# Kernel tuning notes

Hardware: AMD Instinct MI355X
Metric: run time of the kernel (lower is better)

The kernel has to match this reference:

```python
import jax, jax.numpy as jnp
import numpy as np

B, S, E, H = 2, 4096, 768, 12
D = E // H  # head_dim = 64
SCALE = D ** -0.5
NEG = -1e9


def setup_inputs() -> dict:
    key = jax.random.key(0)
    ks = jax.random.split(key, 10)
    init = lambda k, shape: jax.random.normal(k, shape, dtype=jnp.float32) * (shape[-1] ** -0.5)
    x = jax.random.normal(ks[0], (B, S, E), dtype=jnp.float32)
    attention_mask = jnp.zeros((B, 1, S, S), dtype=jnp.float32)
    # additive causal mask: 0 on/below diagonal, -1e9 above
    causal = jnp.where(jnp.tril(jnp.ones((S, S), dtype=bool)), 0.0, NEG).astype(jnp.float32)
    causal_attention_mask = causal[None, None]
    return {
        "x": x,
        "attention_mask": attention_mask,
        "causal_attention_mask": causal_attention_mask,
        "Wq": init(ks[1], (E, E)), "bq": jnp.zeros((E,), jnp.float32),
        "Wk": init(ks[2], (E, E)), "bk": jnp.zeros((E,), jnp.float32),
        "Wv": init(ks[3], (E, E)), "bv": jnp.zeros((E,), jnp.float32),
        "Wo": init(ks[4], (E, E)), "bo": jnp.zeros((E,), jnp.float32),
    }


def _split_heads(t):
    # [B,S,E] -> [B,H,S,D]
    return t.reshape(B, S, H, D).transpose(0, 2, 1, 3)


def reference(x, attention_mask, causal_attention_mask, Wq, bq, Wk, bk, Wv, bv, Wo, bo):
    q = _split_heads(x @ Wq.T + bq)
    k = _split_heads(x @ Wk.T + bk)
    v = _split_heads(x @ Wv.T + bv)
    mask = attention_mask + causal_attention_mask  # [B,1,S,S]
    scores = jnp.einsum("bhqd,bhkd->bhqk", q, k) * SCALE + mask
    probs = jax.nn.softmax(scores.astype(jnp.float32), axis=-1).astype(q.dtype)
    out = jnp.einsum("bhqk,bhkd->bhqd", probs, v)
    out = out.transpose(0, 2, 1, 3).reshape(B, S, E)
    return out @ Wo.T + bo
```

## Files before the change

kernel.cpp:

```cpp
#include <hip/hip_runtime.h>
#include <hip/hip_bf16.h>
#include <stdint.h>

#define B_ 2
#define S_ 4096
#define E_ 768
#define H_ 12
#define D_ 64
#define M_TOT (B_*S_)
#define NQKV (3*E_)

typedef __attribute__((ext_vector_type(8)))  short bf16x8;
typedef __attribute__((ext_vector_type(4)))  float f32x4;
typedef __attribute__((ext_vector_type(16))) float f32x16;
typedef unsigned short u16;
typedef unsigned int   u32;

__device__ __forceinline__ u16 f2bf(float f) {
  __hip_bfloat16 h = __float2bfloat16(f);
  return *reinterpret_cast<u16*>(&h);
}

__device__ __forceinline__ float bf2f(u16 u) {
  union { u32 i; float f; } v; v.i = ((u32)u) << 16; return v.f;
}

__device__ __forceinline__ u32 cvtpk(float lo, float hi) {
  u32 r;
  asm("v_cvt_pk_bf16_f32 %0, %1, %2" : "=v"(r) : "v"(lo), "v"(hi));
  return r;
}

#define GLDS(gp, lp) __builtin_amdgcn_global_load_lds( \
    (const __attribute__((address_space(1))) void*)(gp), \
    (__attribute__((address_space(3))) void*)(lp), 16, 0, 0)

#define QSCALE 0.1803368801111573f


__global__ void k_cast_x(const float* __restrict__ x, u16* __restrict__ xb) {
  int i = blockIdx.x * blockDim.x + threadIdx.x;
  float4 v = reinterpret_cast<const float4*>(x)[i];
  ushort4 o;
  o.x = f2bf(v.x); o.y = f2bf(v.y); o.z = f2bf(v.z); o.w = f2bf(v.w);
  reinterpret_cast<ushort4*>(xb)[i] = o;
}

__global__ void k_pack_wqkv(const float* __restrict__ Wq, const float* __restrict__ Wk,
                            const float* __restrict__ Wv, const float* __restrict__ bq,
                            const float* __restrict__ bk, const float* __restrict__ bv,
                            u16* __restrict__ wqkv, float* __restrict__ bqkv) {
  int i = blockIdx.x * blockDim.x + threadIdx.x;
  int base = i * 4;
  int n = base / E_;
  int k = base % E_;
  const float* src; float sc;
  if (n < E_)        { src = Wq + (size_t)n*E_ + k;        sc = QSCALE; }
  else if (n < 2*E_) { src = Wk + (size_t)(n-E_)*E_ + k;   sc = 1.f; }
  else               { src = Wv + (size_t)(n-2*E_)*E_ + k; sc = 1.f; }
  float4 v = *reinterpret_cast<const float4*>(src);
  ushort4 o;
  o.x = f2bf(v.x*sc); o.y = f2bf(v.y*sc); o.z = f2bf(v.z*sc); o.w = f2bf(v.w*sc);
  reinterpret_cast<ushort4*>(wqkv)[i] = o;
  if (i < NQKV) {
    float b = (i < E_) ? bq[i]*QSCALE : (i < 2*E_) ? bk[i-E_] : bv[i-2*E_];
    bqkv[i] = b;
  }
}

__global__ void k_cast_wo(const float* __restrict__ Wo, u16* __restrict__ wo) {
  int i = blockIdx.x * blockDim.x + threadIdx.x;
  float4 v = reinterpret_cast<const float4*>(Wo)[i];
  ushort4 o;
  o.x = f2bf(v.x); o.y = f2bf(v.y); o.z = f2bf(v.z); o.w = f2bf(v.w);
  reinterpret_cast<ushort4*>(wo)[i] = o;
}


template<int MODE>
__global__ __launch_bounds__(256)
void k_gemm(const u16* __restrict__ A, const u16* __restrict__ W,
            const float* __restrict__ bias,
            u16* __restrict__ dq, u16* __restrict__ dk, u16* __restrict__ dv,
            float* __restrict__ fout)
{
  constexpr int BN = (MODE == 0) ? 128 : 64;
  constexpr int NF = BN / 32;
  __shared__ u16 As[128*64];
  __shared__ u16 Ws[BN*64];
  const int tid  = threadIdx.x;
  const int lane = tid & 63, wave = tid >> 6;
  const int m0 = blockIdx.x * 128;
  const int n0 = blockIdx.y * BN;
  const int g  = lane >> 4, cc = lane & 15;
  const int wr = (wave >> 1) * 64, wc = (wave & 1) * (BN/2);
  const int srow = lane >> 3;
  const int scol = (lane & 7) * 8;

  f32x4 acc[4][NF];
  #pragma unroll
  for (int m = 0; m < 4; ++m)
    #pragma unroll
    for (int n = 0; n < NF; ++n) acc[m][n] = (f32x4){0.f,0.f,0.f,0.f};

  for (int k0 = 0; k0 < E_; k0 += 64) {
    __syncthreads();
    #pragma unroll
    for (int i = 0; i < 4; ++i) {
      const int r0 = (i*4 + wave) * 8;
      GLDS(A + (size_t)(m0 + r0 + srow)*E_ + k0 + scol, As + r0*64);
    }
    #pragma unroll
    for (int i = 0; i < BN/32; ++i) {
      const int r0 = (i*4 + wave) * 8;
      GLDS(W + (size_t)(n0 + r0 + srow)*E_ + k0 + scol, Ws + r0*64);
    }
    __syncthreads();
    #pragma unroll
    for (int kk = 0; kk < 64; kk += 32) {
      bf16x8 af[4], bfr[NF];
      #pragma unroll
      for (int m = 0; m < 4; ++m)
        af[m] = *reinterpret_cast<const bf16x8*>(As + (wr + m*16 + cc)*64 + kk + g*8);
      #pragma unroll
      for (int n = 0; n < NF; ++n)
        bfr[n] = *reinterpret_cast<const bf16x8*>(Ws + (wc + n*16 + cc)*64 + kk + g*8);
      #pragma unroll
      for (int m = 0; m < 4; ++m)
        #pragma unroll
        for (int n = 0; n < NF; ++n)
          acc[m][n] = __builtin_amdgcn_mfma_f32_16x16x32_bf16(af[m], bfr[n], acc[m][n], 0, 0, 0);
    }
  }

  #pragma unroll
  for (int n = 0; n < NF; ++n) {
    const int colg = n0 + wc + n*16 + cc;
    const float bb = bias[colg];
    if (MODE == 0) {
      const int which = colg / E_;
      const int nn = colg % E_;
      const int h = nn >> 6, d = nn & 63;
      #pragma unroll
      for (int m = 0; m < 4; ++m)
        #pragma unroll
        for (int j = 0; j < 4; ++j) {
          const int row = m0 + wr + m*16 + g*4 + j;
          const int b = row >> 12, s = row & (S_-1);
          const u16 val = f2bf(acc[m][n][j] + bb);
          if (which == 0)       dq[(((size_t)b*H_ + h)*S_ + s)*D_ + d] = val;
          else if (which == 1)  dk[(((size_t)b*H_ + h)*S_ + s)*D_ + d] = val;
          else                  dv[(((size_t)b*H_ + h)*D_ + d)*S_ + s] = val;
        }
    } else {
      #pragma unroll
      for (int m = 0; m < 4; ++m)
        #pragma unroll
        for (int j = 0; j < 4; ++j) {
          const int row = m0 + wr + m*16 + g*4 + j;
          fout[(size_t)row*E_ + colg] = acc[m][n][j] + bb;
        }
    }
  }
}


__global__ __launch_bounds__(256, 3)
void k_attn(const u16* __restrict__ Qb, const u16* __restrict__ Kb,
            const u16* __restrict__ Vtg, u16* __restrict__ AO,
            u16* __restrict__ PO, float2* __restrict__ PML)
{
  __shared__ u16 Ks[2][32*128];
  __shared__ u16 Vs[2][32*128];
  const int tid = threadIdx.x, lane = tid & 63, w = tid >> 6;

  const int L    = blockIdx.x;
  const int slot = L >> 8;
  const int cu   = L & 255;
  const int x    = cu & 7;
  const int c    = cu >> 3;
  int r;
  if (slot < 4) r = slot*32 + ((slot & 1) ? (31 - c) : c);
  else          r = 128 + c;
  int head, qt, mode;
  if (r < 120) {
    const int g_ = r / 15, o = r % 15;
    if (o < 9) {
      if (o < 3) { head = o; qt = 15 - g_; mode = 0; }
      else { const int hh = o - 3; head = hh >> 1; mode = 1 + (hh & 1); qt = 31 - 2*g_; }
    } else { const int hh = o - 9; head = hh >> 1; mode = 1 + (hh & 1); qt = 30 - 2*g_; }
  } else {
    const int rr = r - 120; qt = 7 - rr/3; head = rr % 3; mode = 0;
  }
  const int bh = x*3 + head;
  const int q0 = qt * 128;
  const int nt = (mode == 0) ? (2*qt + 2) : (qt + 1);
  const int kvtb = (mode == 2) ? (qt + 1) : 0;

  const size_t kbase = (size_t)bh * S_ * D_;
  const size_t vbase = (size_t)bh * D_ * S_;
  const int hi = lane >> 5, l31 = lane & 31;
  const int swz = (lane & 15) << 4;
  const int qg = q0 + w*32 + l31;

  int stA[2], stB[2];
  #pragma unroll
  for (int i = 0; i < 2; ++i) {
    const int jj = 2*w + i;
    const int row = jj*4 + (lane >> 4);
    const int gb = ((lane & 15) * 16) ^ ((row & 15) << 4);
    stA[i] = row + 32*(gb >> 7);
    stB[i] = (gb & 127) >> 1;
  }

  bf16x8 qf[4];
  #pragma unroll
  for (int ds = 0; ds < 4; ++ds)
    qf[ds] = *reinterpret_cast<const bf16x8*>(Qb + kbase + (size_t)qg*D_ + ds*16 + hi*8);

  const bf16x8 ones = {(short)0x3F80, (short)0x3F80, (short)0x3F80, (short)0x3F80,
                       (short)0x3F80, (short)0x3F80, (short)0x3F80, (short)0x3F80};

  float m_run = 0.f;
  f32x16 o0, o1, cin, lacc;
  #pragma unroll
  for (int r2 = 0; r2 < 16; ++r2) { o0[r2] = 0.f; o1[r2] = 0.f; cin[r2] = 0.f; lacc[r2] = 0.f; }

#define STAGE(buf, kv0_) do { \
    _Pragma("unroll") \
    for (int i = 0; i < 2; ++i) { \
      GLDS(Kb  + kbase + (size_t)((kv0_) + stA[i])*D_ + stB[i], &Ks[buf][(2*w+i)*512]); \
      GLDS(Vtg + vbase + (size_t)stA[i]*S_ + (kv0_) + stB[i],   &Vs[buf][(2*w+i)*512]); \
    } } while(0)

  int cur = 0;
  STAGE(0, kvtb*64);

  for (int it = 0; it < nt; ++it) {
    asm volatile("s_waitcnt vmcnt(0)" ::: "memory");
    __builtin_amdgcn_s_barrier();
    asm volatile("" ::: "memory");
    if (it + 1 < nt) STAGE(cur ^ 1, (kvtb + it + 1)*64);

    const int kvt = kvtb + it;
    const int kv0 = kvt * 64;
    const u16* bK = Ks[cur];
    const u16* bV = Vs[cur];

    f32x16 s0, s1;
    __builtin_amdgcn_s_setprio(1);
    {
      const int off = (16*hi ^ swz) >> 1;
      bf16x8 a0 = *reinterpret_cast<const bf16x8*>(bK + l31*128 + off);
      bf16x8 a1 = *reinterpret_cast<const bf16x8*>(bK + l31*128 + (off ^ 64));
      s0 = __builtin_amdgcn_mfma_f32_32x32x16_bf16(a0, qf[0], cin, 0, 0, 0);
      s1 = __builtin_amdgcn_mfma_f32_32x32x16_bf16(a1, qf[0], cin, 0, 0, 0);
    }
    #pragma unroll
    for (int ds = 1; ds < 4; ++ds) {
      const int off = ((32*ds + 16*hi) ^ swz) >> 1;
      bf16x8 a0 = *reinterpret_cast<const bf16x8*>(bK + l31*128 + off);
      bf16x8 a1 = *reinterpret_cast<const bf16x8*>(bK + l31*128 + (off ^ 64));
      s0 = __builtin_amdgcn_mfma_f32_32x32x16_bf16(a0, qf[ds], s0, 0, 0, 0);
      s1 = __builtin_amdgcn_mfma_f32_32x32x16_bf16(a1, qf[ds], s1, 0, 0, 0);
    }
    __builtin_amdgcn_s_setprio(0);

    if (kvt >= 2*qt) {
      #pragma unroll
      for (int r2 = 0; r2 < 16; ++r2) {
        const int kvl = kv0 + (r2&3) + 8*(r2>>2) + 4*hi;
        s0[r2] = (kvl      > qg) ? -1e30f : s0[r2];
        s1[r2] = (kvl + 32 > qg) ? -1e30f : s1[r2];
      }
    }

    #pragma unroll
    for (int r2 = 0; r2 < 16; ++r2) s0[r2] = exp2f(s0[r2]);
    #pragma unroll
    for (int r2 = 0; r2 < 16; ++r2) s1[r2] = exp2f(s1[r2]);

    u32 c16[16];
    #pragma unroll
    for (int i = 0; i < 8; ++i) {
      c16[i]   = cvtpk(s0[2*i], s0[2*i+1]);
      c16[8+i] = cvtpk(s1[2*i], s1[2*i+1]);
    }

    #pragma unroll
    for (int ks = 0; ks < 4; ++ks) {
      const int cb = (ks>>1)*8 + (ks&1)*4;
      u32 x0 = c16[cb],   y0 = c16[cb+2];
      u32 x1 = c16[cb+1], y1 = c16[cb+3];
      asm volatile("v_permlane32_swap_b32 %0, %1" : "+v"(x0), "+v"(y0));
      asm volatile("v_permlane32_swap_b32 %0, %1" : "+v"(x1), "+v"(y1));
      union { u32 u[4]; bf16x8 v; } pf;
      pf.u[0] = x0; pf.u[1] = x1; pf.u[2] = y0; pf.u[3] = y1;
      const int voff = ((32*ks + 16*hi) ^ swz) >> 1;
      bf16x8 v0 = *reinterpret_cast<const bf16x8*>(bV + l31*128 + voff);
      bf16x8 v1 = *reinterpret_cast<const bf16x8*>(bV + l31*128 + (voff ^ 64));
      __builtin_amdgcn_s_setprio(1);
      o0   = __builtin_amdgcn_mfma_f32_32x32x16_bf16(v0,   pf.v, o0,   0, 0, 0);
      o1   = __builtin_amdgcn_mfma_f32_32x32x16_bf16(v1,   pf.v, o1,   0, 0, 0);
      lacc = __builtin_amdgcn_mfma_f32_32x32x16_bf16(ones, pf.v, lacc, 0, 0, 0);
      __builtin_amdgcn_s_setprio(0);
    }

    if (!__all(lacc[0] <= 1073741824.0f)) {
      const float alpha = 0x1p-40f;
      m_run += 40.f;
      #pragma unroll
      for (int r2 = 0; r2 < 16; ++r2) {
        o0[r2] *= alpha; o1[r2] *= alpha; lacc[r2] *= alpha;
        cin[r2] -= 40.f;
      }
    }

    cur ^= 1;
  }
#undef STAGE

  const float l_run = lacc[0];
  if (mode == 0) {
    const int b = bh / H_, h = bh % H_;
    const float inv = 1.0f / l_run;
    u16* dst = AO + ((size_t)b*S_ + qg)*E_ + h*64;
    #pragma unroll
    for (int aa = 0; aa < 4; ++aa) {
      ushort4 wv;
      wv.x = f2bf(o0[4*aa+0]*inv); wv.y = f2bf(o0[4*aa+1]*inv);
      wv.z = f2bf(o0[4*aa+2]*inv); wv.w = f2bf(o0[4*aa+3]*inv);
      *reinterpret_cast<ushort4*>(dst + aa*8 + hi*4) = wv;
    }
    #pragma unroll
    for (int aa = 0; aa < 4; ++aa) {
      ushort4 wv;
      wv.x = f2bf(o1[4*aa+0]*inv); wv.y = f2bf(o1[4*aa+1]*inv);
      wv.z = f2bf(o1[4*aa+2]*inv); wv.w = f2bf(o1[4*aa+3]*inv);
      *reinterpret_cast<ushort4*>(dst + 32 + aa*8 + hi*4) = wv;
    }
  } else {
    const int qslot = (bh*16 + (qt-16))*2 + (mode - 1);
    const int rowt = w*32 + l31;
    u16* po = PO + (size_t)qslot*(128*64) + rowt*64;
    #pragma unroll
    for (int aa = 0; aa < 4; ++aa) {
      ushort4 wv;
      wv.x = f2bf(o0[4*aa+0]); wv.y = f2bf(o0[4*aa+1]);
      wv.z = f2bf(o0[4*aa+2]); wv.w = f2bf(o0[4*aa+3]);
      *reinterpret_cast<ushort4*>(po + aa*8 + hi*4) = wv;
    }
    #pragma unroll
    for (int aa = 0; aa < 4; ++aa) {
      ushort4 wv;
      wv.x = f2bf(o1[4*aa+0]); wv.y = f2bf(o1[4*aa+1]);
      wv.z = f2bf(o1[4*aa+2]); wv.w = f2bf(o1[4*aa+3]);
      *reinterpret_cast<ushort4*>(po + 32 + aa*8 + hi*4) = wv;
    }
    if (hi == 0) PML[qslot*128 + rowt] = make_float2(m_run, l_run);
  }
}


__global__ __launch_bounds__(256)
void k_comb(const u16* __restrict__ PO, const float2* __restrict__ PML,
            u16* __restrict__ AO)
{
  const int bid = blockIdx.x;
  const int bh = bid >> 4, qi = bid & 15, q = 16 + qi;
  const int t = threadIdx.x;
  const int r = t >> 1, half = t & 1;
  const int s0 = (bh*16 + qi)*2, s1 = s0 + 1;
  const float2 ml0 = PML[s0*128 + r];
  const float2 ml1 = PML[s1*128 + r];
  const float mstar = fmaxf(ml0.x, ml1.x);
  const float w0 = exp2f(ml0.x - mstar);
  const float w1 = exp2f(ml1.x - mstar);
  const float inv = 1.0f / (ml0.y*w0 + ml1.y*w1);
  const float a0 = w0 * inv, a1 = w1 * inv;
  const u16* p0 = PO + (size_t)s0*(128*64) + r*64 + half*32;
  const u16* p1 = PO + (size_t)s1*(128*64) + r*64 + half*32;
  const int b = bh / H_, h = bh % H_;
  const int row = q*128 + r;
  u16* dst = AO + ((size_t)b*S_ + row)*E_ + h*64 + half*32;
  #pragma unroll
  for (int i = 0; i < 4; ++i) {
    bf16x8 v0 = *reinterpret_cast<const bf16x8*>(p0 + i*8);
    bf16x8 v1 = *reinterpret_cast<const bf16x8*>(p1 + i*8);
    ushort4 lo, hi4;
    float f0 = bf2f(((const u16*)&v0)[0])*a0 + bf2f(((const u16*)&v1)[0])*a1;
    float f1 = bf2f(((const u16*)&v0)[1])*a0 + bf2f(((const u16*)&v1)[1])*a1;
    float f2 = bf2f(((const u16*)&v0)[2])*a0 + bf2f(((const u16*)&v1)[2])*a1;
    float f3 = bf2f(((const u16*)&v0)[3])*a0 + bf2f(((const u16*)&v1)[3])*a1;
    lo.x = f2bf(f0); lo.y = f2bf(f1); lo.z = f2bf(f2); lo.w = f2bf(f3);
    float f4 = bf2f(((const u16*)&v0)[4])*a0 + bf2f(((const u16*)&v1)[4])*a1;
    float f5 = bf2f(((const u16*)&v0)[5])*a0 + bf2f(((const u16*)&v1)[5])*a1;
    float f6 = bf2f(((const u16*)&v0)[6])*a0 + bf2f(((const u16*)&v1)[6])*a1;
    float f7 = bf2f(((const u16*)&v0)[7])*a0 + bf2f(((const u16*)&v1)[7])*a1;
    hi4.x = f2bf(f4); hi4.y = f2bf(f5); hi4.z = f2bf(f6); hi4.w = f2bf(f7);
    *reinterpret_cast<ushort4*>(dst + i*8)     = lo;
    *reinterpret_cast<ushort4*>(dst + i*8 + 4) = hi4;
  }
}


extern "C" void kernel_launch(void* const* d_in, const int* in_sizes, int n_in,
                              void* d_out, int out_size, void* d_ws, size_t ws_size,
                              hipStream_t stream) {
  const float* x  = (const float*)d_in[0];
  const float* Wq = (const float*)d_in[3];
  const float* bq = (const float*)d_in[4];
  const float* Wk = (const float*)d_in[5];
  const float* bk = (const float*)d_in[6];
  const float* Wv = (const float*)d_in[7];
  const float* bv = (const float*)d_in[8];
  const float* Wo = (const float*)d_in[9];
  const float* bo = (const float*)d_in[10];
  float* out = (float*)d_out;

  const size_t SZ_X   = (size_t)M_TOT * E_ * 2;
  const size_t SZ_WQKV= (size_t)NQKV * E_ * 2;
  const size_t SZ_WO  = (size_t)E_ * E_ * 2;
  const size_t SZ_B   = (size_t)NQKV * 4;
  char* w = (char*)d_ws;
  u16*   xb   = (u16*)(w);
  u16*   wqkv = (u16*)(w + SZ_X);
  u16*   wob  = (u16*)(w + SZ_X + SZ_WQKV);
  float* bqkv = (float*)(w + SZ_X + SZ_WQKV + SZ_WO);
  char*  w2   = w + SZ_X + SZ_WQKV + SZ_WO + SZ_B;
  u16* Qb = (u16*)(w2);
  u16* Kb = (u16*)(w2 + SZ_X);
  u16* Vb = (u16*)(w2 + 2*SZ_X);
  u16* AO = (u16*)(w2 + 3*SZ_X);
  u16* PO = xb;
  float2* PML = (float2*)(w2 + 4*SZ_X);

  k_cast_x  <<<6144, 256, 0, stream>>>(x, xb);
  k_pack_wqkv<<<1728, 256, 0, stream>>>(Wq, Wk, Wv, bq, bk, bv, wqkv, bqkv);
  k_cast_wo <<<576,  256, 0, stream>>>(Wo, wob);

  dim3 gq(64, 18);
  k_gemm<0><<<gq, 256, 0, stream>>>(xb, wqkv, bqkv, Qb, Kb, Vb, nullptr);

  k_attn<<<1152, 256, 0, stream>>>(Qb, Kb, Vb, AO, PO, PML);
  k_comb<<<384, 256, 0, stream>>>(PO, PML, AO);

  dim3 go(64, 12);
  k_gemm<1><<<go, 256, 0, stream>>>(AO, wob, bo, nullptr, nullptr, nullptr, out);
}
```

Before: 201.9 us.

## Use stream-K style equal-work partitioning for causal attention blocks

```diff
diff --git a/kernel.cpp b/kernel.cpp
--- a/kernel.cpp
+++ b/kernel.cpp
@@ -168,84 +168,84 @@
 __global__ __launch_bounds__(256, 3)
 void k_attn(const u16* __restrict__ Qb, const u16* __restrict__ Kb,
             const u16* __restrict__ Vtg, u16* __restrict__ AO,
-            u16* __restrict__ PO, float2* __restrict__ PML)
+            u16* __restrict__ PO, float2* __restrict__ PMLA,
+            float2* __restrict__ PMLB)
 {
   __shared__ u16 Ks[2][32*128];
   __shared__ u16 Vs[2][32*128];
-  const int tid = threadIdx.x, lane = tid & 63, w = tid >> 6;
-
-  const int L    = blockIdx.x;
-  const int slot = L >> 8;
-  const int cu   = L & 255;
-  const int x    = cu & 7;
-  const int c    = cu >> 3;
-  int r;
-  if (slot < 4) r = slot*32 + ((slot & 1) ? (31 - c) : c);
-  else          r = 128 + c;
-  int head, qt, mode;
-  if (r < 120) {
-    const int g_ = r / 15, o = r % 15;
-    if (o < 9) {
-      if (o < 3) { head = o; qt = 15 - g_; mode = 0; }
-      else { const int hh = o - 3; head = hh >> 1; mode = 1 + (hh & 1); qt = 31 - 2*g_; }
-    } else { const int hh = o - 9; head = hh >> 1; mode = 1 + (hh & 1); qt = 30 - 2*g_; }
-  } else {
-    const int rr = r - 120; qt = 7 - rr/3; head = rr % 3; mode = 0;
-  }
-  const int bh = x*3 + head;
-  const int q0 = qt * 128;
-  const int nt = (mode == 0) ? (2*qt + 2) : (qt + 1);
-  const int kvtb = (mode == 2) ? (qt + 1) : 0;
+  const int tid = threadIdx.x, lane = tid & 63, wv = tid >> 6;
+
+  const int L  = blockIdx.x;
+  const int x  = L & 7;
+  const int g  = L >> 3;
+  const int h  = g >> 5;
+  const int qh = g & 31;
+  const int bh = x*3 + h;
+  const int b_ = bh / H_, h_ = bh % H_;
 
   const size_t kbase = (size_t)bh * S_ * D_;
   const size_t vbase = (size_t)bh * D_ * S_;
   const int hi = lane >> 5, l31 = lane & 31;
   const int swz = (lane & 15) << 4;
-  const int qg = q0 + w*32 + l31;
 
   int stA[2], stB[2];
   #pragma unroll
   for (int i = 0; i < 2; ++i) {
-    const int jj = 2*w + i;
+    const int jj = 2*wv + i;
     const int row = jj*4 + (lane >> 4);
     const int gb = ((lane & 15) * 16) ^ ((row & 15) << 4);
     stA[i] = row + 32*(gb >> 7);
     stB[i] = (gb & 127) >> 1;
   }
 
-  bf16x8 qf[4];
-  #pragma unroll
-  for (int ds = 0; ds < 4; ++ds)
-    qf[ds] = *reinterpret_cast<const bf16x8*>(Qb + kbase + (size_t)qg*D_ + ds*16 + hi*8);
+  const int lw0 = 33*qh;
+  int qt = (int)((sqrtf(4.0f*lw0 + 1.0f) - 1.0f) * 0.5f);
+  while ((qt+1)*(qt+2) <= lw0) ++qt;
+  while (qt*qt + qt > lw0) --qt;
+  int kv = lw0 - (qt*qt + qt);
+  bool headSeg = (kv == 0);
 
   const bf16x8 ones = {(short)0x3F80, (short)0x3F80, (short)0x3F80, (short)0x3F80,
                        (short)0x3F80, (short)0x3F80, (short)0x3F80, (short)0x3F80};
 
-  float m_run = 0.f;
+  bf16x8 qf[4];
+  float m_run;
   f32x16 o0, o1, cin, lacc;
-  #pragma unroll
-  for (int r2 = 0; r2 < 16; ++r2) { o0[r2] = 0.f; o1[r2] = 0.f; cin[r2] = 0.f; lacc[r2] = 0.f; }
-
-#define STAGE(buf, kv0_) do { \
+
+#define LOADQ(qtc) do { \
+    const int qg_ = (qtc)*128 + wv*32 + l31; \
+    _Pragma("unroll") \
+    for (int ds = 0; ds < 4; ++ds) \
+      qf[ds] = *reinterpret_cast<const bf16x8*>(Qb + kbase + (size_t)qg_*D_ + ds*16 + hi*8); \
+    m_run = 0.f; \
+    _Pragma("unroll") \
+    for (int r2 = 0; r2 < 16; ++r2) { o0[r2]=0.f; o1[r2]=0.f; cin[r2]=0.f; lacc[r2]=0.f; } \
+  } while(0)
+
+#define STAGE(buf, kvt_) do { \
     _Pragma("unroll") \
     for (int i = 0; i < 2; ++i) { \
-      GLDS(Kb  + kbase + (size_t)((kv0_) + stA[i])*D_ + stB[i], &Ks[buf][(2*w+i)*512]); \
-      GLDS(Vtg + vbase + (size_t)stA[i]*S_ + (kv0_) + stB[i],   &Vs[buf][(2*w+i)*512]); \
+      GLDS(Kb  + kbase + (size_t)((kvt_)*64 + stA[i])*D_ + stB[i], &Ks[buf][(2*wv+i)*512]); \
+      GLDS(Vtg + vbase + (size_t)stA[i]*S_ + (kvt_)*64 + stB[i],   &Vs[buf][(2*wv+i)*512]); \
     } } while(0)
 
+  LOADQ(qt);
+  STAGE(0, kv);
   int cur = 0;
-  STAGE(0, kvtb*64);
-
-  for (int it = 0; it < nt; ++it) {
+
+  for (int it = 0; it < 33; ++it) {
+    const bool tailSeg = (kv == 2*qt + 1);
+    const int qtn = tailSeg ? qt + 1 : qt;
+    const int kvn = tailSeg ? 0 : kv + 1;
+
     asm volatile("s_waitcnt vmcnt(0)" ::: "memory");
     __builtin_amdgcn_s_barrier();
     asm volatile("" ::: "memory");
-    if (it + 1 < nt) STAGE(cur ^ 1, (kvtb + it + 1)*64);
-
-    const int kvt = kvtb + it;
-    const int kv0 = kvt * 64;
+    if (it + 1 < 33) STAGE(cur ^ 1, kvn);
+
     const u16* bK = Ks[cur];
     const u16* bV = Vs[cur];
+    const int qg = qt*128 + wv*32 + l31;
 
     f32x16 s0, s1;
     __builtin_amdgcn_s_setprio(1);
@@ -266,7 +266,8 @@
     }
     __builtin_amdgcn_s_setprio(0);
 
-    if (kvt >= 2*qt) {
+    if (kv >= 2*qt) {
+      const int kv0 = kv * 64;
       #pragma unroll
       for (int r2 = 0; r2 < 16; ++r2) {
         const int kvl = kv0 + (r2&3) + 8*(r2>>2) + 4*hi;
@@ -316,88 +317,118 @@
       }
     }
 
-    cur ^= 1;
+    if (tailSeg || it == 32) {
+      const float l_run = lacc[0];
+      if (headSeg && tailSeg) {
+        const float inv = 1.0f / l_run;
+        u16* dst = AO + ((size_t)b_*S_ + qg)*E_ + h_*64;
+        #pragma unroll
+        for (int aa = 0; aa < 4; ++aa) {
+          ushort4 wvc;
+          wvc.x = f2bf(o0[4*aa+0]*inv); wvc.y = f2bf(o0[4*aa+1]*inv);
+          wvc.z = f2bf(o0[4*aa+2]*inv); wvc.w = f2bf(o0[4*aa+3]*inv);
+          *reinterpret_cast<ushort4*>(dst + aa*8 + hi*4) = wvc;
+        }
+        #pragma unroll
+        for (int aa = 0; aa < 4; ++aa) {
+          ushort4 wvc;
+          wvc.x = f2bf(o1[4*aa+0]*inv); wvc.y = f2bf(o1[4*aa+1]*inv);
+          wvc.z = f2bf(o1[4*aa+2]*inv); wvc.w = f2bf(o1[4*aa+3]*inv);
+          *reinterpret_cast<ushort4*>(dst + 32 + aa*8 + hi*4) = wvc;
+        }
+      } else {
+        u16* po;
+        if (headSeg) {
+          po = AO + ((size_t)b_*S_ + qg)*E_ + h_*64;
+          if (hi == 0) PMLA[(bh*32 + qt)*128 + wv*32 + l31] = make_float2(m_run, l_run);
+        } else {
+          po = PO + (size_t)L*(128*64) + (wv*32 + l31)*64;
+          if (hi == 0) PMLB[L*128 + wv*32 + l31] = make_float2(m_run, l_run);
+        }
+        #pragma unroll
+        for (int aa = 0; aa < 4; ++aa) {
+          ushort4 wvc;
+          wvc.x = f2bf(o0[4*aa+0]); wvc.y = f2bf(o0[4*aa+1]);
+          wvc.z = f2bf(o0[4*aa+2]); wvc.w = f2bf(o0[4*aa+3]);
+          *reinterpret_cast<ushort4*>(po + aa*8 + hi*4) = wvc;
+        }
+        #pragma unroll
+        for (int aa = 0; aa < 4; ++aa) {
+          ushort4 wvc;
+          wvc.x = f2bf(o1[4*aa+0]); wvc.y = f2bf(o1[4*aa+1]);
+          wvc.z = f2bf(o1[4*aa+2]); wvc.w = f2bf(o1[4*aa+3]);
+          *reinterpret_cast<ushort4*>(po + 32 + aa*8 + hi*4) = wvc;
+        }
+      }
+      if (tailSeg && it < 32) { LOADQ(qtn); headSeg = true; }
+    }
+    qt = qtn; kv = kvn; cur ^= 1;
   }
 #undef STAGE
-
-  const float l_run = lacc[0];
-  if (mode == 0) {
-    const int b = bh / H_, h = bh % H_;
-    const float inv = 1.0f / l_run;
-    u16* dst = AO + ((size_t)b*S_ + qg)*E_ + h*64;
-    #pragma unroll
-    for (int aa = 0; aa < 4; ++aa) {
-      ushort4 wv;
-      wv.x = f2bf(o0[4*aa+0]*inv); wv.y = f2bf(o0[4*aa+1]*inv);
-      wv.z = f2bf(o0[4*aa+2]*inv); wv.w = f2bf(o0[4*aa+3]*inv);
-      *reinterpret_cast<ushort4*>(dst + aa*8 + hi*4) = wv;
-    }
-    #pragma unroll
-    for (int aa = 0; aa < 4; ++aa) {
-      ushort4 wv;
-      wv.x = f2bf(o1[4*aa+0]*inv); wv.y = f2bf(o1[4*aa+1]*inv);
-      wv.z = f2bf(o1[4*aa+2]*inv); wv.w = f2bf(o1[4*aa+3]*inv);
-      *reinterpret_cast<ushort4*>(dst + 32 + aa*8 + hi*4) = wv;
-    }
-  } else {
-    const int qslot = (bh*16 + (qt-16))*2 + (mode - 1);
-    const int rowt = w*32 + l31;
-    u16* po = PO + (size_t)qslot*(128*64) + rowt*64;
-    #pragma unroll
-    for (int aa = 0; aa < 4; ++aa) {
-      ushort4 wv;
-      wv.x = f2bf(o0[4*aa+0]); wv.y = f2bf(o0[4*aa+1]);
-      wv.z = f2bf(o0[4*aa+2]); wv.w = f2bf(o0[4*aa+3]);
-      *reinterpret_cast<ushort4*>(po + aa*8 + hi*4) = wv;
-    }
-    #pragma unroll
-    for (int aa = 0; aa < 4; ++aa) {
-      ushort4 wv;
-      wv.x = f2bf(o1[4*aa+0]); wv.y = f2bf(o1[4*aa+1]);
-      wv.z = f2bf(o1[4*aa+2]); wv.w = f2bf(o1[4*aa+3]);
-      *reinterpret_cast<ushort4*>(po + 32 + aa*8 + hi*4) = wv;
-    }
-    if (hi == 0) PML[qslot*128 + rowt] = make_float2(m_run, l_run);
-  }
+#undef LOADQ
 }
 
 
 __global__ __launch_bounds__(256)
-void k_comb(const u16* __restrict__ PO, const float2* __restrict__ PML,
-            u16* __restrict__ AO)
+void k_comb(const u16* __restrict__ PO, const float2* __restrict__ PMLA,
+            const float2* __restrict__ PMLB, u16* __restrict__ AO)
 {
-  const int bid = blockIdx.x;
-  const int bh = bid >> 4, qi = bid & 15, q = 16 + qi;
-  const int t = threadIdx.x;
-  const int r = t >> 1, half = t & 1;
-  const int s0 = (bh*16 + qi)*2, s1 = s0 + 1;
-  const float2 ml0 = PML[s0*128 + r];
-  const float2 ml1 = PML[s1*128 + r];
-  const float mstar = fmaxf(ml0.x, ml1.x);
-  const float w0 = exp2f(ml0.x - mstar);
-  const float w1 = exp2f(ml1.x - mstar);
-  const float inv = 1.0f / (ml0.y*w0 + ml1.y*w1);
-  const float a0 = w0 * inv, a1 = w1 * inv;
-  const u16* p0 = PO + (size_t)s0*(128*64) + r*64 + half*32;
-  const u16* p1 = PO + (size_t)s1*(128*64) + r*64 + half*32;
-  const int b = bh / H_, h = bh % H_;
-  const int row = q*128 + r;
-  u16* dst = AO + ((size_t)b*S_ + row)*E_ + h*64 + half*32;
+  const int L = blockIdx.x;
+  const int x = L & 7, g = L >> 3, h = g >> 5, k = g & 31;
+  if (k == 0) return;
+  const int lw0 = 33*k;
+  int qt = (int)((sqrtf(4.0f*lw0 + 1.0f) - 1.0f) * 0.5f);
+  while ((qt+1)*(qt+2) <= lw0) ++qt;
+  while (qt*qt + qt > lw0) --qt;
+  const int ws = qt*qt + qt;
+  if (lw0 == ws) return;
+  const int kA = ws / 33;
+  if (k != kA + 1) return;
+  const int we = ws + 2*qt + 2;
+  const int ncut = (we - 1)/33 - kA;
+  const int bh = x*3 + h;
+  const int b_ = bh / H_, h_ = bh % H_;
+  const int t = threadIdx.x, r = t >> 1, half = t & 1;
+
+  float m[3], l[3];
+  { float2 ml = PMLA[(bh*32 + qt)*128 + r]; m[0] = ml.x; l[0] = ml.y; }
+  int Ls[3];
+  for (int j = 1; j <= ncut; ++j) {
+    Ls[j] = ((h*32 + kA + j) << 3) | x;
+    float2 ml = PMLB[Ls[j]*128 + r]; m[j] = ml.x; l[j] = ml.y;
+  }
+  float mstar = m[0];
+  for (int j = 1; j <= ncut; ++j) mstar = fmaxf(mstar, m[j]);
+  float wgt[3], wsum = 0.f;
+  for (int j = 0; j <= ncut; ++j) { wgt[j] = exp2f(m[j] - mstar); wsum += l[j]*wgt[j]; }
+  const float inv = 1.0f / wsum;
+
+  const int row = qt*128 + r;
+  u16* dst = AO + ((size_t)b_*S_ + row)*E_ + h_*64 + half*32;
+
+  float acc[32];
   #pragma unroll
   for (int i = 0; i < 4; ++i) {
-    bf16x8 v0 = *reinterpret_cast<const bf16x8*>(p0 + i*8);
-    bf16x8 v1 = *reinterpret_cast<const bf16x8*>(p1 + i*8);
+    bf16x8 v = *reinterpret_cast<const bf16x8*>(dst + i*8);
+    #pragma unroll
+    for (int e = 0; e < 8; ++e) acc[i*8+e] = bf2f(((const u16*)&v)[e]) * wgt[0];
+  }
+  for (int j = 1; j <= ncut; ++j) {
+    const u16* p = PO + (size_t)Ls[j]*(128*64) + r*64 + half*32;
+    #pragma unroll
+    for (int i = 0; i < 4; ++i) {
+      bf16x8 v = *reinterpret_cast<const bf16x8*>(p + i*8);
+      #pragma unroll
+      for (int e = 0; e < 8; ++e) acc[i*8+e] += bf2f(((const u16*)&v)[e]) * wgt[j];
+    }
+  }
+  #pragma unroll
+  for (int i = 0; i < 4; ++i) {
     ushort4 lo, hi4;
-    float f0 = bf2f(((const u16*)&v0)[0])*a0 + bf2f(((const u16*)&v1)[0])*a1;
-    float f1 = bf2f(((const u16*)&v0)[1])*a0 + bf2f(((const u16*)&v1)[1])*a1;
-    float f2 = bf2f(((const u16*)&v0)[2])*a0 + bf2f(((const u16*)&v1)[2])*a1;
-    float f3 = bf2f(((const u16*)&v0)[3])*a0 + bf2f(((const u16*)&v1)[3])*a1;
-    lo.x = f2bf(f0); lo.y = f2bf(f1); lo.z = f2bf(f2); lo.w = f2bf(f3);
-    float f4 = bf2f(((const u16*)&v0)[4])*a0 + bf2f(((const u16*)&v1)[4])*a1;
-    float f5 = bf2f(((const u16*)&v0)[5])*a0 + bf2f(((const u16*)&v1)[5])*a1;
-    float f6 = bf2f(((const u16*)&v0)[6])*a0 + bf2f(((const u16*)&v1)[6])*a1;
-    float f7 = bf2f(((const u16*)&v0)[7])*a0 + bf2f(((const u16*)&v1)[7])*a1;
-    hi4.x = f2bf(f4); hi4.y = f2bf(f5); hi4.z = f2bf(f6); hi4.w = f2bf(f7);
+    lo.x = f2bf(acc[i*8+0]*inv); lo.y = f2bf(acc[i*8+1]*inv);
+    lo.z = f2bf(acc[i*8+2]*inv); lo.w = f2bf(acc[i*8+3]*inv);
+    hi4.x = f2bf(acc[i*8+4]*inv); hi4.y = f2bf(acc[i*8+5]*inv);
+    hi4.z = f2bf(acc[i*8+6]*inv); hi4.w = f2bf(acc[i*8+7]*inv);
     *reinterpret_cast<ushort4*>(dst + i*8)     = lo;
     *reinterpret_cast<ushort4*>(dst + i*8 + 4) = hi4;
   }
@@ -433,7 +464,8 @@
   u16* Vb = (u16*)(w2 + 2*SZ_X);
   u16* AO = (u16*)(w2 + 3*SZ_X);
   u16* PO = xb;
-  float2* PML = (float2*)(w2 + 4*SZ_X);
+  float2* PMLA = (float2*)(w2 + 4*SZ_X);
+  float2* PMLB = PMLA + 768*128;
 
   k_cast_x  <<<6144, 256, 0, stream>>>(x, xb);
   k_pack_wqkv<<<1728, 256, 0, stream>>>(Wq, Wk, Wv, bq, bk, bv, wqkv, bqkv);
@@ -442,8 +474,8 @@
   dim3 gq(64, 18);
   k_gemm<0><<<gq, 256, 0, stream>>>(xb, wqkv, bqkv, Qb, Kb, Vb, nullptr);
 
-  k_attn<<<1152, 256, 0, stream>>>(Qb, Kb, Vb, AO, PO, PML);
-  k_comb<<<384, 256, 0, stream>>>(PO, PML, AO);
+  k_attn<<<768, 256, 0, stream>>>(Qb, Kb, Vb, AO, PO, PMLA, PMLB);
+  k_comb<<<768, 256, 0, stream>>>(PO, PMLA, PMLB, AO);
 
   dim3 go(64, 12);
   k_gemm<1><<<go, 256, 0, stream>>>(AO, wob, bo, nullptr, nullptr, nullptr, out);
```

Result: slower. 218.6 us (+8.3%).
